# Kernel tuning notes

Measured on AMD Instinct MI355X. Metric: run time of the kernel, lower is better.

The kernel has to match this reference:

```python
import jax, jax.numpy as jnp
import numpy as np

N_WIRES = 8
DIM = 2 ** N_WIRES  # 256
N_OPS = 20

# Fixed realization of tq.RandomLayer(n_ops=20): ops drawn once with a fixed seed.
_rs = np.random.RandomState(0)
RAND_OPS = []
for _ in range(N_OPS):
    k = int(_rs.randint(4))
    if k == 3:
        c, t = _rs.choice(N_WIRES, 2, replace=False)
        RAND_OPS.append(("cnot", int(c), int(t)))
    else:
        RAND_OPS.append((("rx", "ry", "rz")[k], int(_rs.randint(N_WIRES)), 0))

_idx = np.arange(DIM)
# Z eigenvalue sign per wire per basis state (wire 0 = most significant bit)
ZSIGN_NP = np.stack([1.0 - 2.0 * ((_idx >> (N_WIRES - 1 - w)) & 1) for w in range(N_WIRES)]).astype(np.float32)
ZSIGN = jnp.asarray(ZSIGN_NP)        # [8, 256]
ZS_T = jnp.asarray(ZSIGN_NP.T)       # [256, 8]

# CNOT is a basis permutation: precompute index maps for each cnot op.
PERMS = {}
for _i, _op in enumerate(RAND_OPS):
    if _op[0] == "cnot":
        _c, _t = _op[1], _op[2]
        _cb = (_idx >> (N_WIRES - 1 - _c)) & 1
        PERMS[_i] = jnp.asarray(_idx ^ (_cb << (N_WIRES - 1 - _t)))


def _ry_mat(t):
    c = jnp.cos(t * 0.5).astype(jnp.complex64)
    s = jnp.sin(t * 0.5).astype(jnp.complex64)
    return jnp.stack([jnp.stack([c, -s]), jnp.stack([s, c])])


def _rx_mat(t):
    c = jnp.cos(t * 0.5).astype(jnp.complex64)
    s = (-1j * jnp.sin(t * 0.5)).astype(jnp.complex64)
    return jnp.stack([jnp.stack([c, s]), jnp.stack([s, c])])


def _apply_1q(state, U, w):
    # state: [B, 256]; apply 2x2 U on wire w
    B = state.shape[0]
    s = state.reshape(B, 2 ** w, 2, -1)
    return jnp.einsum('ij,bajc->baic', U, s).reshape(B, DIM)


def _forward(x, ry_theta, rand_params, W1, b1, W2, b2):
    B, S, E = x.shape
    f = x.reshape(B * S, E)[:, :N_WIRES]  # encoder uses input_idx 0..7
    # Encoder: RY(f_w) on |0> for each wire -> product state, built by kron chain
    c = jnp.cos(f * 0.5)
    s = jnp.sin(f * 0.5)
    state = jnp.ones((B * S, 1), jnp.float32)
    for w in range(N_WIRES):
        v = jnp.stack([c[:, w], s[:, w]], axis=-1)  # [BS, 2]
        state = (state[:, :, None] * v[:, None, :]).reshape(B * S, -1)
    state = state.astype(jnp.complex64)  # [BS, 256]
    # Fixed random layer
    for i, op in enumerate(RAND_OPS):
        kind = op[0]
        if kind == "cnot":
            state = state[:, PERMS[i]]
        elif kind == "rz":
            ph = jnp.exp((-0.5j * rand_params[i]) * ZSIGN[op[1]]).astype(jnp.complex64)
            state = state * ph[None, :]
        elif kind == "rx":
            state = _apply_1q(state, _rx_mat(rand_params[i]), op[1])
        else:
            state = _apply_1q(state, _ry_mat(rand_params[i]), op[1])
    # Trainable per-wire RY gates
    for w in range(N_WIRES):
        state = _apply_1q(state, _ry_mat(ry_theta[w]), w)
    # MeasureAll(PauliZ): <Z_w> = sum_b |amp_b|^2 * zsign_w(b)
    probs = (state.real ** 2 + state.imag ** 2)  # [BS, 256] float32
    expv = probs @ ZS_T                          # [BS, 8]
    h = jax.nn.relu(expv @ W1.T + b1)
    out = h @ W2.T + b2
    return out.reshape(B, S, -1)


def setup_inputs() -> dict:
    key = jax.random.key(0)
    k1, k2, k3, k4, k5 = jax.random.split(key, 5)
    B, S, E = 4, 4096, 512
    pi = 3.14159265
    x = jax.random.normal(k1, (B, S, E), jnp.float32)
    ry_theta = jax.random.uniform(k2, (N_WIRES,), jnp.float32, -pi, pi)
    rand_params = jax.random.uniform(k3, (N_OPS,), jnp.float32, -pi, pi)
    W1 = jax.random.normal(k4, (64, N_WIRES), jnp.float32) * (1.0 / np.sqrt(N_WIRES))
    b1 = jnp.zeros((64,), jnp.float32)
    W2 = jax.random.normal(k5, (E, 64), jnp.float32) * (1.0 / 8.0)
    b2 = jnp.zeros((E,), jnp.float32)
    return {"x": x, "ry_theta": ry_theta, "rand_params": rand_params, "W1": W1, "b1": b1, "W2": W2, "b2": b2}


def reference(x, ry_theta, rand_params, W1, b1, W2, b2):
    return _forward(x, ry_theta, rand_params, W1, b1, W2, b2)
```

## Files before the change

### kernel.cpp

```cpp
#include <hip/hip_runtime.h>
#include <hip/hip_fp16.h>
#include <cstdint>

#define N_RAND   20
#define N_GATES  28
#define E_DIM    512

struct OpsArg { int d[N_GATES]; };

struct MT19937ce {
  uint32_t mt[624] = {};
  int mti = 0;
  constexpr void seed(uint32_t s){
    mt[0]=s;
    for(int i=1;i<624;i++) mt[i]=1812433253u*(mt[i-1]^(mt[i-1]>>30))+(uint32_t)i;
    mti=624;
  }
  constexpr uint32_t next(){
    if(mti>=624){
      for(int i=0;i<624;i++){
        uint32_t y=(mt[i]&0x80000000u)|(mt[(i+1)%624]&0x7fffffffu);
        mt[i]=mt[(i+397)%624]^(y>>1)^((y&1u)?0x9908b0dfu:0u);
      }
      mti=0;
    }
    uint32_t y=mt[mti++];
    y^=y>>11; y^=(y<<7)&0x9d2c5680u; y^=(y<<15)&0xefc60000u; y^=y>>18;
    return y;
  }
  constexpr uint32_t interval(uint32_t mx){
    if(!mx) return 0;
    uint32_t mask=mx; mask|=mask>>1; mask|=mask>>2; mask|=mask>>4; mask|=mask>>8; mask|=mask>>16;
    uint32_t v = next()&mask;
    while(v>mx) v = next()&mask;
    return v;
  }
};

constexpr OpsArg build_ops_ce(){
  MT19937ce rs; rs.seed(0);
  OpsArg o{};
  for(int i=0;i<N_RAND;i++){
    uint32_t k = rs.interval(3);
    if(k==3){
      int perm[8] = {0,1,2,3,4,5,6,7};
      for(int j=7;j>=1;j--){
        uint32_t t=rs.interval((uint32_t)j);
        int tmp=perm[j]; perm[j]=perm[t]; perm[t]=tmp;
      }
      o.d[i] = 3 | (perm[0]<<2) | (perm[1]<<5);
    } else {
      uint32_t w = rs.interval(7);
      o.d[i] = (int)k | ((int)w<<2);
    }
  }
  for(int i=0;i<8;i++) o.d[N_RAND+i] = 1 | (i<<2);
  return o;
}
inline constexpr OpsArg OPS = build_ops_ce();

__device__ __forceinline__ float readlane_f(float v, int l){
  return __int_as_float(__builtin_amdgcn_readlane(__float_as_int(v), l));
}
template<int CTRL>
__device__ __forceinline__ float dpp_mov(float v){
  int s = __float_as_int(v);
  return __int_as_float(__builtin_amdgcn_update_dpp(s, s, CTRL, 0xF, 0xF, false));
}
template<int M>
__device__ __forceinline__ float xl(float v){
  if constexpr (M==1)      return dpp_mov<0xB1>(v);
  else if constexpr (M==2) return dpp_mov<0x4E>(v);
  else return __int_as_float(__builtin_amdgcn_ds_swizzle(__float_as_int(v), (M<<10)|0x1F));
}
template<int L>
__device__ __forceinline__ float bcast(float v){
  return __int_as_float(__builtin_amdgcn_ds_swizzle(__float_as_int(v), L<<5));
}

typedef _Float16 v2h __attribute__((ext_vector_type(2)));
typedef _Float16 v8h __attribute__((ext_vector_type(8)));
typedef float    v4f __attribute__((ext_vector_type(4)));
union HU  { uint32_t u; v2h h; };

template<int G>
__device__ __forceinline__ void run_gates(float (&ar)[8], float (&ai)[8],
                                          const float (&sgn)[5], int l,
                                          float cv, float sv)
{
  if constexpr (G < N_GATES){
    constexpr int dd   = OPS.d[G];
    constexpr int kind = dd & 3;
    constexpr int wa   = (dd>>2) & 7;
    constexpr int wb   = (dd>>5) & 7;
    const float gc = readlane_f(cv, G);
    const float gs = readlane_f(sv, G);

    if constexpr (kind == 3){
      if constexpr (wa < 3 && wb < 3){
        constexpr int Rc = 4>>wa, Rt = 4>>wb;
        #pragma unroll
        for (int r=0;r<8;r++){
          if ((r & Rc) && !(r & Rt)){
            float t0=ar[r]; ar[r]=ar[r|Rt]; ar[r|Rt]=t0;
            float t1=ai[r]; ai[r]=ai[r|Rt]; ai[r|Rt]=t1;
          }
        }
      } else if constexpr (wa < 3){
        constexpr int Rc = 4>>wa, Mt = 16>>(wb-3);
        #pragma unroll
        for (int r=0;r<8;r++){
          if (r & Rc){ ar[r]=xl<Mt>(ar[r]); ai[r]=xl<Mt>(ai[r]); }
        }
      } else if constexpr (wb < 3){
        constexpr int Mc = 16>>(wa-3), Rt = 4>>wb;
        const bool cb = (l & Mc) != 0;
        #pragma unroll
        for (int r=0;r<8;r++){
          if (!(r & Rt)){
            float alo=ar[r], ahi=ar[r|Rt];
            ar[r]    = cb ? ahi : alo;  ar[r|Rt] = cb ? alo : ahi;
            float blo=ai[r], bhi=ai[r|Rt];
            ai[r]    = cb ? bhi : blo;  ai[r|Rt] = cb ? blo : bhi;
          }
        }
      } else {
        constexpr int Mc = 16>>(wa-3), Mt = 16>>(wb-3);
        const bool cb = (l & Mc) != 0;
        #pragma unroll
        for (int r=0;r<8;r++){
          float pr = xl<Mt>(ar[r]), pi_ = xl<Mt>(ai[r]);
          ar[r] = cb ? pr  : ar[r];
          ai[r] = cb ? pi_ : ai[r];
        }
      }
    } else if constexpr (kind == 2){
      if constexpr (wa < 3){
        constexpr int Rb = 4>>wa;
        #pragma unroll
        for (int r=0;r<8;r++){
          const float pim = (r & Rb) ? gs : -gs;
          float nr = gc*ar[r] - pim*ai[r];
          ai[r] = gc*ai[r] + pim*ar[r];
          ar[r] = nr;
        }
      } else {
        constexpr int SI = wa-3;
        const float pim = sgn[SI]*gs;
        #pragma unroll
        for (int r=0;r<8;r++){
          float nr = gc*ar[r] - pim*ai[r];
          ai[r] = gc*ai[r] + pim*ar[r];
          ar[r] = nr;
        }
      }
    } else if constexpr (kind == 1){
      if constexpr (wa < 3){
        constexpr int Rb = 4>>wa;
        #pragma unroll
        for (int r=0;r<8;r++){
          if (!(r & Rb)){
            const int h = r|Rb;
            float lr=ar[r], li=ai[r], hr=ar[h], hii=ai[h];
            ar[r]=gc*lr - gs*hr;  ai[r]=gc*li - gs*hii;
            ar[h]=gs*lr + gc*hr;  ai[h]=gs*li + gc*hii;
          }
        }
      } else {
        constexpr int M = 16>>(wa-3), SI = wa-3;
        const float sg = sgn[SI]*gs;
        #pragma unroll
        for (int r=0;r<8;r++){
          float pr = xl<M>(ar[r]), pi_ = xl<M>(ai[r]);
          ar[r] = gc*ar[r] + sg*pr;
          ai[r] = gc*ai[r] + sg*pi_;
        }
      }
    } else {
      if constexpr (wa < 3){
        constexpr int Rb = 4>>wa;
        #pragma unroll
        for (int r=0;r<8;r++){
          if (!(r & Rb)){
            const int h = r|Rb;
            float lr=ar[r], li=ai[r], hr=ar[h], hii=ai[h];
            ar[r]=gc*lr + gs*hii;  ai[r]=gc*li - gs*hr;
            ar[h]=gc*hr + gs*li;   ai[h]=gc*hii - gs*lr;
          }
        }
      } else {
        constexpr int M = 16>>(wa-3);
        #pragma unroll
        for (int r=0;r<8;r++){
          float pr = xl<M>(ar[r]), pi_ = xl<M>(ai[r]);
          ar[r] = gc*ar[r] + gs*pi_;
          ai[r] = gc*ai[r] - gs*pr;
        }
      }
    }
    run_gates<G+1>(ar, ai, sgn, l, cv, sv);
  }
}

__global__ __launch_bounds__(512)
void qffb_pre(const float* __restrict__ ry_theta,
              const float* __restrict__ rand_params,
              _Float16* __restrict__ Urf,
              _Float16* __restrict__ Uif)
{
  const int tid  = threadIdx.x;
  const int lane = tid & 63;
  const int l    = lane & 31;
  const int wave = tid >> 6;
  const int b    = blockIdx.x*16 + wave*2 + (lane>>5);

  float th = 0.f;
  if (lane < N_GATES)
    th = (lane < N_RAND) ? rand_params[lane] : ry_theta[lane - N_RAND];
  float cv, sv;
  __sincosf(0.5f*th, &sv, &cv);

  float sgn[5];
  sgn[0] = (l&16) ? 1.f : -1.f;
  sgn[1] = (l& 8) ? 1.f : -1.f;
  sgn[2] = (l& 4) ? 1.f : -1.f;
  sgn[3] = (l& 2) ? 1.f : -1.f;
  sgn[4] = (l& 1) ? 1.f : -1.f;

  float ar[8], ai[8];
  #pragma unroll
  for (int r=0;r<8;r++){
    ar[r] = (((b>>5)==r) && ((b&31)==l)) ? 1.f : 0.f;
    ai[r] = 0.f;
  }

  run_gates<0>(ar, ai, sgn, l, cv, sv);

  const int k  = b >> 5;
  const int qd = (b >> 3) & 3;
  const int jj = b & 7;
  #pragma unroll
  for (int r=0;r<8;r++){
    const int j   = r*32 + l;
    const int nt  = j >> 4;
    const int rr_ = j & 15;
    const size_t F = ((size_t)((nt*8 + k)*4 + qd)*16 + rr_)*8 + jj;
    Urf[F] = (_Float16)ar[r];
    Uif[F] = (_Float16)ai[r];
  }
}

#define PSTRIDE 272
#define PFSTR   264
__global__ __launch_bounds__(512)
void qffb_main(const float* __restrict__ x,
               const _Float16* __restrict__ Urf,
               const _Float16* __restrict__ Uif,
               const float* __restrict__ W1,
               const float* __restrict__ b1,
               const float* __restrict__ W2,
               const float* __restrict__ b2,
               float* __restrict__ out)
{
  __shared__ _Float16 Ps[16*PSTRIDE];
  __shared__ _Float16 Hs[16][72];
  __shared__ float    Ts[8][16*68];
  float* Pf = &Ts[0][0];

  const int tid  = threadIdx.x;
  const int lane = tid & 63;
  const int l    = lane & 31;
  const int wave = tid >> 6;
  const int rr   = lane & 15;
  const int quad = lane >> 4;
  const int trow = wave*2 + (lane>>5);
  const int token = blockIdx.x*16 + trow;

  {
    const float4 xa = *(const float4*)(x + (size_t)token*E_DIM);
    const float4 xb = *(const float4*)(x + (size_t)token*E_DIM + 4);
    float c[8], s[8];
    float xs[8] = {xa.x, xa.y, xa.z, xa.w, xb.x, xb.y, xb.z, xb.w};
    #pragma unroll
    for (int w=0; w<8; ++w) __sincosf(0.5f*xs[w], &s[w], &c[w]);
    float L = ((l&16)? s[0]:c[0]) * ((l&8)? s[1]:c[1]);
    L *= ((l&4)? s[2]:c[2]) * ((l&2)? s[3]:c[3]);
    L *= ((l&1)? s[4]:c[4]);
    const float p67[4] = {c[6]*c[7], c[6]*s[7], s[6]*c[7], s[6]*s[7]};
    v8h v;
    #pragma unroll
    for (int i=0;i<8;++i)
      v[i] = (_Float16)(L * (((i&4)? s[5]:c[5]) * p67[i&3]));
    *(v8h*)&Ps[trow*PSTRIDE + l*8] = v;
  }
  __syncthreads();

  v4f accr[2], acci[2];
  #pragma unroll
  for (int n=0;n<2;++n){ accr[n]=v4f{0.f,0.f,0.f,0.f}; acci[n]=v4f{0.f,0.f,0.f,0.f}; }

  const size_t ub0 = ((size_t)((wave*2+0)*32 + quad)*16 + rr)*8;
  const size_t ub1 = ((size_t)((wave*2+1)*32 + quad)*16 + rr)*8;

  v8h br0 = *(const v8h*)(Urf + ub0);
  v8h bi0 = *(const v8h*)(Uif + ub0);
  v8h br1 = *(const v8h*)(Urf + ub1);
  v8h bi1 = *(const v8h*)(Uif + ub1);

  #pragma unroll
  for (int k=0;k<8;++k){
    v8h nbr0, nbi0, nbr1, nbi1;
    if (k < 7){
      const size_t o = (size_t)(k+1)*512;
      nbr0 = *(const v8h*)(Urf + ub0 + o);
      nbi0 = *(const v8h*)(Uif + ub0 + o);
      nbr1 = *(const v8h*)(Urf + ub1 + o);
      nbi1 = *(const v8h*)(Uif + ub1 + o);
    }
    const v8h a0 = *(const v8h*)&Ps[rr*PSTRIDE + k*32 + quad*8];
    accr[0] = __builtin_amdgcn_mfma_f32_16x16x32_f16(a0, br0, accr[0], 0,0,0);
    acci[0] = __builtin_amdgcn_mfma_f32_16x16x32_f16(a0, bi0, acci[0], 0,0,0);
    accr[1] = __builtin_amdgcn_mfma_f32_16x16x32_f16(a0, br1, accr[1], 0,0,0);
    acci[1] = __builtin_amdgcn_mfma_f32_16x16x32_f16(a0, bi1, acci[1], 0,0,0);
    if (k < 7){ br0=nbr0; bi0=nbi0; br1=nbr1; bi1=nbi1; }
  }

  #pragma unroll
  for (int n=0;n<2;++n){
    const int nt = wave*2 + n;
    #pragma unroll
    for (int r2=0;r2<4;++r2)
      Pf[(quad*4+r2)*PFSTR + nt*16 + rr] =
          accr[n][r2]*accr[n][r2] + acci[n][r2]*acci[n][r2];
  }
  __syncthreads();

  float sgn[5];
  sgn[0] = (l&16) ? 1.f : -1.f;
  sgn[1] = (l& 8) ? 1.f : -1.f;
  sgn[2] = (l& 4) ? 1.f : -1.f;
  sgn[3] = (l& 2) ? 1.f : -1.f;
  sgn[4] = (l& 1) ? 1.f : -1.f;

  float p[8];
  #pragma unroll
  for (int r=0;r<8;r++) p[r] = Pf[trow*PFSTR + r*32 + l];

  const float t1a=p[0]+p[1], t1b=p[2]+p[3], t1c=p[4]+p[5], t1d=p[6]+p[7];
  const float s0a=t1a+t1b, s0b=t1c+t1d;
  float P  = s0a + s0b;
  float e0 = s0a - s0b;
  float e1 = (t1a+t1c) - (t1b+t1d);
  float e2 = (p[0]-p[1])+(p[2]-p[3])+(p[4]-p[5])+(p[6]-p[7]);
  {
    float t;
    t=xl<1>(e0); e0+=t;  t=xl<1>(e1); e1+=t;  t=xl<1>(e2); e2+=t;
    t=xl<1>(P);  P = fmaf(-sgn[4], P, t);
    t=xl<2>(e0); e0+=t;  t=xl<2>(e1); e1+=t;  t=xl<2>(e2); e2+=t;
    t=xl<2>(P);  P = fmaf(-sgn[3], P, t);
    t=xl<4>(e0); e0+=t;  t=xl<4>(e1); e1+=t;  t=xl<4>(e2); e2+=t;
    t=xl<4>(P);  P = fmaf(-sgn[2], P, t);
    t=xl<8>(e0); e0+=t;  t=xl<8>(e1); e1+=t;  t=xl<8>(e2); e2+=t;
    t=xl<8>(P);  P = fmaf(-sgn[1], P, t);
    t=xl<16>(e0); e0+=t; t=xl<16>(e1); e1+=t; t=xl<16>(e2); e2+=t;
    t=xl<16>(P); P = fmaf(-sgn[0], P, t);
  }
  const float e3 = bcast<16>(P);
  const float e4 = bcast<8>(P);
  const float e5 = bcast<4>(P);
  const float e6 = bcast<2>(P);
  const float e7 = bcast<1>(P);

  {
    const float4 wA0 = *(const float4*)(W1 + (size_t)(2*l)*8);
    const float4 wA1 = *(const float4*)(W1 + (size_t)(2*l)*8 + 4);
    const float4 wB0 = *(const float4*)(W1 + (size_t)(2*l+1)*8);
    const float4 wB1 = *(const float4*)(W1 + (size_t)(2*l+1)*8 + 4);
    const float2 bb  = *(const float2*)(b1 + 2*l);
    float h0 = bb.x + wA0.x*e0 + wA0.y*e1 + wA0.z*e2 + wA0.w*e3
                    + wA1.x*e4 + wA1.y*e5 + wA1.z*e6 + wA1.w*e7;
    float h1 = bb.y + wB0.x*e0 + wB0.y*e1 + wB0.z*e2 + wB0.w*e3
                    + wB1.x*e4 + wB1.y*e5 + wB1.z*e6 + wB1.w*e7;
    HU pk;
    pk.h = v2h{(_Float16)fmaxf(h0,0.f), (_Float16)fmaxf(h1,0.f)};
    *(uint32_t*)((char*)&Hs[trow][0] + 4*l) = pk.u;
  }
  __syncthreads();

  const int mt = blockIdx.x;
  const int ng = wave;

  const v8h a0 = *(const v8h*)&Hs[rr][quad*8];
  const v8h a1 = *(const v8h*)&Hs[rr][32 + quad*8];

  #pragma unroll
  for (int j=0;j<4;++j){
    const int e = ng*64 + j*16 + rr;
    const float4 wa = *(const float4*)(W2 + (size_t)e*64 + quad*8);
    const float4 wb = *(const float4*)(W2 + (size_t)e*64 + quad*8 + 4);
    const float4 wc = *(const float4*)(W2 + (size_t)e*64 + 32 + quad*8);
    const float4 wd = *(const float4*)(W2 + (size_t)e*64 + 32 + quad*8 + 4);
    const v8h b0 = v8h{(_Float16)wa.x,(_Float16)wa.y,(_Float16)wa.z,(_Float16)wa.w,
                      (_Float16)wb.x,(_Float16)wb.y,(_Float16)wb.z,(_Float16)wb.w};
    const v8h b1v = v8h{(_Float16)wc.x,(_Float16)wc.y,(_Float16)wc.z,(_Float16)wc.w,
                      (_Float16)wd.x,(_Float16)wd.y,(_Float16)wd.z,(_Float16)wd.w};
    v4f acc = {0.f,0.f,0.f,0.f};
    acc = __builtin_amdgcn_mfma_f32_16x16x32_f16(a0, b0, acc, 0, 0, 0);
    acc = __builtin_amdgcn_mfma_f32_16x16x32_f16(a1, b1v, acc, 0, 0, 0);
    #pragma unroll
    for (int r2=0;r2<4;r2++)
      Ts[wave][(quad*4+r2)*68 + j*16 + rr] = acc[r2];
  }

  const float4 bias = *(const float4*)(b2 + ng*64 + rr*4);
  #pragma unroll
  for (int k=0;k<4;++k){
    const int row = 4*k + quad;
    float4 v = *(const float4*)&Ts[wave][row*68 + rr*4];
    v.x += bias.x; v.y += bias.y; v.z += bias.z; v.w += bias.w;
    const int t = mt*16 + row;
    *(float4*)(out + (size_t)t*E_DIM + ng*64 + rr*4) = v;
  }
}

extern "C" void kernel_launch(void* const* d_in, const int* in_sizes, int n_in,
                              void* d_out, int out_size, void* d_ws, size_t ws_size,
                              hipStream_t stream)
{
  (void)n_in; (void)out_size; (void)ws_size;
  const int ntok = in_sizes[0] / E_DIM;
  char* ws = (char*)d_ws;
  _Float16* Urf = (_Float16*)(ws);
  _Float16* Uif = (_Float16*)(ws + 131072);

  qffb_pre<<<16, 512, 0, stream>>>(
      (const float*)d_in[1],
      (const float*)d_in[2],
      Urf, Uif);

  qffb_main<<<ntok/16, 512, 0, stream>>>(
      (const float*)d_in[0],
      Urf, Uif,
      (const float*)d_in[3],
      (const float*)d_in[4],
      (const float*)d_in[5],
      (const float*)d_in[6],
      (float*)d_out);
}
```

Before: 121.8 us.

## Process four token tiles per block and keep U and W2 in registers

Each block now loops over four 16-token tiles. The unitary B-fragments, W1/b1, the fp16-converted W2 fragments and the b2 bias are loaded once into registers before the loop and reused for every tile. The grid shrinks by four, cutting redundant global loads and fp32-to-fp16 conversion of the weights per block. In exchange register pressure rises considerably, fewer blocks are resident to hide latency, and the tiles inside a block run serially with barriers between stages.

Result: faster. 109.3 us (-10.3%).

```diff
diff --git a/kernel.cpp b/kernel.cpp
--- a/kernel.cpp
+++ b/kernel.cpp
@@ -5,6 +5,7 @@
 #define N_RAND   20
 #define N_GATES  28
 #define E_DIM    512
+#define TPB_TILES 4
 
 struct OpsArg { int d[N_GATES]; };
 
@@ -274,66 +275,18 @@
   const int rr   = lane & 15;
   const int quad = lane >> 4;
   const int trow = wave*2 + (lane>>5);
-  const int token = blockIdx.x*16 + trow;
-
-  {
-    const float4 xa = *(const float4*)(x + (size_t)token*E_DIM);
-    const float4 xb = *(const float4*)(x + (size_t)token*E_DIM + 4);
-    float c[8], s[8];
-    float xs[8] = {xa.x, xa.y, xa.z, xa.w, xb.x, xb.y, xb.z, xb.w};
-    #pragma unroll
-    for (int w=0; w<8; ++w) __sincosf(0.5f*xs[w], &s[w], &c[w]);
-    float L = ((l&16)? s[0]:c[0]) * ((l&8)? s[1]:c[1]);
-    L *= ((l&4)? s[2]:c[2]) * ((l&2)? s[3]:c[3]);
-    L *= ((l&1)? s[4]:c[4]);
-    const float p67[4] = {c[6]*c[7], c[6]*s[7], s[6]*c[7], s[6]*s[7]};
-    v8h v;
-    #pragma unroll
-    for (int i=0;i<8;++i)
-      v[i] = (_Float16)(L * (((i&4)? s[5]:c[5]) * p67[i&3]));
-    *(v8h*)&Ps[trow*PSTRIDE + l*8] = v;
-  }
-  __syncthreads();
-
-  v4f accr[2], acci[2];
-  #pragma unroll
-  for (int n=0;n<2;++n){ accr[n]=v4f{0.f,0.f,0.f,0.f}; acci[n]=v4f{0.f,0.f,0.f,0.f}; }
 
   const size_t ub0 = ((size_t)((wave*2+0)*32 + quad)*16 + rr)*8;
   const size_t ub1 = ((size_t)((wave*2+1)*32 + quad)*16 + rr)*8;
-
-  v8h br0 = *(const v8h*)(Urf + ub0);
-  v8h bi0 = *(const v8h*)(Uif + ub0);
-  v8h br1 = *(const v8h*)(Urf + ub1);
-  v8h bi1 = *(const v8h*)(Uif + ub1);
-
+  v8h Br0[8], Bi0[8], Br1[8], Bi1[8];
   #pragma unroll
   for (int k=0;k<8;++k){
-    v8h nbr0, nbi0, nbr1, nbi1;
-    if (k < 7){
-      const size_t o = (size_t)(k+1)*512;
-      nbr0 = *(const v8h*)(Urf + ub0 + o);
-      nbi0 = *(const v8h*)(Uif + ub0 + o);
-      nbr1 = *(const v8h*)(Urf + ub1 + o);
-      nbi1 = *(const v8h*)(Uif + ub1 + o);
-    }
-    const v8h a0 = *(const v8h*)&Ps[rr*PSTRIDE + k*32 + quad*8];
-    accr[0] = __builtin_amdgcn_mfma_f32_16x16x32_f16(a0, br0, accr[0], 0,0,0);
-    acci[0] = __builtin_amdgcn_mfma_f32_16x16x32_f16(a0, bi0, acci[0], 0,0,0);
-    accr[1] = __builtin_amdgcn_mfma_f32_16x16x32_f16(a0, br1, accr[1], 0,0,0);
-    acci[1] = __builtin_amdgcn_mfma_f32_16x16x32_f16(a0, bi1, acci[1], 0,0,0);
-    if (k < 7){ br0=nbr0; bi0=nbi0; br1=nbr1; bi1=nbi1; }
-  }
-
-  #pragma unroll
-  for (int n=0;n<2;++n){
-    const int nt = wave*2 + n;
-    #pragma unroll
-    for (int r2=0;r2<4;++r2)
-      Pf[(quad*4+r2)*PFSTR + nt*16 + rr] =
-          accr[n][r2]*accr[n][r2] + acci[n][r2]*acci[n][r2];
-  }
-  __syncthreads();
+    const size_t o = (size_t)k*512;
+    Br0[k] = *(const v8h*)(Urf + ub0 + o);
+    Bi0[k] = *(const v8h*)(Uif + ub0 + o);
+    Br1[k] = *(const v8h*)(Urf + ub1 + o);
+    Bi1[k] = *(const v8h*)(Uif + ub1 + o);
+  }
 
   float sgn[5];
   sgn[0] = (l&16) ? 1.f : -1.f;
@@ -342,57 +295,14 @@
   sgn[3] = (l& 2) ? 1.f : -1.f;
   sgn[4] = (l& 1) ? 1.f : -1.f;
 
-  float p[8];
-  #pragma unroll
-  for (int r=0;r<8;r++) p[r] = Pf[trow*PFSTR + r*32 + l];
-
-  const float t1a=p[0]+p[1], t1b=p[2]+p[3], t1c=p[4]+p[5], t1d=p[6]+p[7];
-  const float s0a=t1a+t1b, s0b=t1c+t1d;
-  float P  = s0a + s0b;
-  float e0 = s0a - s0b;
-  float e1 = (t1a+t1c) - (t1b+t1d);
-  float e2 = (p[0]-p[1])+(p[2]-p[3])+(p[4]-p[5])+(p[6]-p[7]);
-  {
-    float t;
-    t=xl<1>(e0); e0+=t;  t=xl<1>(e1); e1+=t;  t=xl<1>(e2); e2+=t;
-    t=xl<1>(P);  P = fmaf(-sgn[4], P, t);
-    t=xl<2>(e0); e0+=t;  t=xl<2>(e1); e1+=t;  t=xl<2>(e2); e2+=t;
-    t=xl<2>(P);  P = fmaf(-sgn[3], P, t);
-    t=xl<4>(e0); e0+=t;  t=xl<4>(e1); e1+=t;  t=xl<4>(e2); e2+=t;
-    t=xl<4>(P);  P = fmaf(-sgn[2], P, t);
-    t=xl<8>(e0); e0+=t;  t=xl<8>(e1); e1+=t;  t=xl<8>(e2); e2+=t;
-    t=xl<8>(P);  P = fmaf(-sgn[1], P, t);
-    t=xl<16>(e0); e0+=t; t=xl<16>(e1); e1+=t; t=xl<16>(e2); e2+=t;
-    t=xl<16>(P); P = fmaf(-sgn[0], P, t);
-  }
-  const float e3 = bcast<16>(P);
-  const float e4 = bcast<8>(P);
-  const float e5 = bcast<4>(P);
-  const float e6 = bcast<2>(P);
-  const float e7 = bcast<1>(P);
-
-  {
-    const float4 wA0 = *(const float4*)(W1 + (size_t)(2*l)*8);
-    const float4 wA1 = *(const float4*)(W1 + (size_t)(2*l)*8 + 4);
-    const float4 wB0 = *(const float4*)(W1 + (size_t)(2*l+1)*8);
-    const float4 wB1 = *(const float4*)(W1 + (size_t)(2*l+1)*8 + 4);
-    const float2 bb  = *(const float2*)(b1 + 2*l);
-    float h0 = bb.x + wA0.x*e0 + wA0.y*e1 + wA0.z*e2 + wA0.w*e3
-                    + wA1.x*e4 + wA1.y*e5 + wA1.z*e6 + wA1.w*e7;
-    float h1 = bb.y + wB0.x*e0 + wB0.y*e1 + wB0.z*e2 + wB0.w*e3
-                    + wB1.x*e4 + wB1.y*e5 + wB1.z*e6 + wB1.w*e7;
-    HU pk;
-    pk.h = v2h{(_Float16)fmaxf(h0,0.f), (_Float16)fmaxf(h1,0.f)};
-    *(uint32_t*)((char*)&Hs[trow][0] + 4*l) = pk.u;
-  }
-  __syncthreads();
-
-  const int mt = blockIdx.x;
+  const float4 wA0 = *(const float4*)(W1 + (size_t)(2*l)*8);
+  const float4 wA1 = *(const float4*)(W1 + (size_t)(2*l)*8 + 4);
+  const float4 wB0 = *(const float4*)(W1 + (size_t)(2*l+1)*8);
+  const float4 wB1 = *(const float4*)(W1 + (size_t)(2*l+1)*8 + 4);
+  const float2 bb  = *(const float2*)(b1 + 2*l);
+
   const int ng = wave;
-
-  const v8h a0 = *(const v8h*)&Hs[rr][quad*8];
-  const v8h a1 = *(const v8h*)&Hs[rr][32 + quad*8];
-
+  v8h WB0[4], WB1[4];
   #pragma unroll
   for (int j=0;j<4;++j){
     const int e = ng*64 + j*16 + rr;
@@ -400,26 +310,122 @@
     const float4 wb = *(const float4*)(W2 + (size_t)e*64 + quad*8 + 4);
     const float4 wc = *(const float4*)(W2 + (size_t)e*64 + 32 + quad*8);
     const float4 wd = *(const float4*)(W2 + (size_t)e*64 + 32 + quad*8 + 4);
-    const v8h b0 = v8h{(_Float16)wa.x,(_Float16)wa.y,(_Float16)wa.z,(_Float16)wa.w,
-                      (_Float16)wb.x,(_Float16)wb.y,(_Float16)wb.z,(_Float16)wb.w};
-    const v8h b1v = v8h{(_Float16)wc.x,(_Float16)wc.y,(_Float16)wc.z,(_Float16)wc.w,
-                      (_Float16)wd.x,(_Float16)wd.y,(_Float16)wd.z,(_Float16)wd.w};
-    v4f acc = {0.f,0.f,0.f,0.f};
-    acc = __builtin_amdgcn_mfma_f32_16x16x32_f16(a0, b0, acc, 0, 0, 0);
-    acc = __builtin_amdgcn_mfma_f32_16x16x32_f16(a1, b1v, acc, 0, 0, 0);
+    WB0[j] = v8h{(_Float16)wa.x,(_Float16)wa.y,(_Float16)wa.z,(_Float16)wa.w,
+                 (_Float16)wb.x,(_Float16)wb.y,(_Float16)wb.z,(_Float16)wb.w};
+    WB1[j] = v8h{(_Float16)wc.x,(_Float16)wc.y,(_Float16)wc.z,(_Float16)wc.w,
+                 (_Float16)wd.x,(_Float16)wd.y,(_Float16)wd.z,(_Float16)wd.w};
+  }
+  const float4 bias = *(const float4*)(b2 + ng*64 + rr*4);
+
+  for (int it=0; it<TPB_TILES; ++it){
+    const int tileIdx = blockIdx.x*TPB_TILES + it;
+    const int token   = tileIdx*16 + trow;
+
+    {
+      const float4 xa = *(const float4*)(x + (size_t)token*E_DIM);
+      const float4 xb = *(const float4*)(x + (size_t)token*E_DIM + 4);
+      float c[8], s[8];
+      float xs[8] = {xa.x, xa.y, xa.z, xa.w, xb.x, xb.y, xb.z, xb.w};
+      #pragma unroll
+      for (int w=0; w<8; ++w) __sincosf(0.5f*xs[w], &s[w], &c[w]);
+      float L = ((l&16)? s[0]:c[0]) * ((l&8)? s[1]:c[1]);
+      L *= ((l&4)? s[2]:c[2]) * ((l&2)? s[3]:c[3]);
+      L *= ((l&1)? s[4]:c[4]);
+      const float p67[4] = {c[6]*c[7], c[6]*s[7], s[6]*c[7], s[6]*s[7]};
+      v8h v;
+      #pragma unroll
+      for (int i=0;i<8;++i)
+        v[i] = (_Float16)(L * (((i&4)? s[5]:c[5]) * p67[i&3]));
+      *(v8h*)&Ps[trow*PSTRIDE + l*8] = v;
+    }
+    __syncthreads();
+
+    v4f accr[2], acci[2];
     #pragma unroll
-    for (int r2=0;r2<4;r2++)
-      Ts[wave][(quad*4+r2)*68 + j*16 + rr] = acc[r2];
-  }
-
-  const float4 bias = *(const float4*)(b2 + ng*64 + rr*4);
-  #pragma unroll
-  for (int k=0;k<4;++k){
-    const int row = 4*k + quad;
-    float4 v = *(const float4*)&Ts[wave][row*68 + rr*4];
-    v.x += bias.x; v.y += bias.y; v.z += bias.z; v.w += bias.w;
-    const int t = mt*16 + row;
-    *(float4*)(out + (size_t)t*E_DIM + ng*64 + rr*4) = v;
+    for (int n=0;n<2;++n){ accr[n]=v4f{0.f,0.f,0.f,0.f}; acci[n]=v4f{0.f,0.f,0.f,0.f}; }
+
+    #pragma unroll
+    for (int k=0;k<8;++k){
+      const v8h a0 = *(const v8h*)&Ps[rr*PSTRIDE + k*32 + quad*8];
+      accr[0] = __builtin_amdgcn_mfma_f32_16x16x32_f16(a0, Br0[k], accr[0], 0,0,0);
+      acci[0] = __builtin_amdgcn_mfma_f32_16x16x32_f16(a0, Bi0[k], acci[0], 0,0,0);
+      accr[1] = __builtin_amdgcn_mfma_f32_16x16x32_f16(a0, Br1[k], accr[1], 0,0,0);
+      acci[1] = __builtin_amdgcn_mfma_f32_16x16x32_f16(a0, Bi1[k], acci[1], 0,0,0);
+    }
+
+    #pragma unroll
+    for (int n=0;n<2;++n){
+      const int nt = wave*2 + n;
+      #pragma unroll
+      for (int r2=0;r2<4;++r2)
+        Pf[(quad*4+r2)*PFSTR + nt*16 + rr] =
+            accr[n][r2]*accr[n][r2] + acci[n][r2]*acci[n][r2];
+    }
+    __syncthreads();
+
+    {
+      float p[8];
+      #pragma unroll
+      for (int r=0;r<8;r++) p[r] = Pf[trow*PFSTR + r*32 + l];
+
+      const float t1a=p[0]+p[1], t1b=p[2]+p[3], t1c=p[4]+p[5], t1d=p[6]+p[7];
+      const float s0a=t1a+t1b, s0b=t1c+t1d;
+      float P  = s0a + s0b;
+      float e0 = s0a - s0b;
+      float e1 = (t1a+t1c) - (t1b+t1d);
+      float e2 = (p[0]-p[1])+(p[2]-p[3])+(p[4]-p[5])+(p[6]-p[7]);
+      {
+        float t;
+        t=xl<1>(e0); e0+=t;  t=xl<1>(e1); e1+=t;  t=xl<1>(e2); e2+=t;
+        t=xl<1>(P);  P = fmaf(-sgn[4], P, t);
+        t=xl<2>(e0); e0+=t;  t=xl<2>(e1); e1+=t;  t=xl<2>(e2); e2+=t;
+        t=xl<2>(P);  P = fmaf(-sgn[3], P, t);
+        t=xl<4>(e0); e0+=t;  t=xl<4>(e1); e1+=t;  t=xl<4>(e2); e2+=t;
+        t=xl<4>(P);  P = fmaf(-sgn[2], P, t);
+        t=xl<8>(e0); e0+=t;  t=xl<8>(e1); e1+=t;  t=xl<8>(e2); e2+=t;
+        t=xl<8>(P);  P = fmaf(-sgn[1], P, t);
+        t=xl<16>(e0); e0+=t; t=xl<16>(e1); e1+=t; t=xl<16>(e2); e2+=t;
+        t=xl<16>(P); P = fmaf(-sgn[0], P, t);
+      }
+      const float e3 = bcast<16>(P);
+      const float e4 = bcast<8>(P);
+      const float e5 = bcast<4>(P);
+      const float e6 = bcast<2>(P);
+      const float e7 = bcast<1>(P);
+
+      float h0 = bb.x + wA0.x*e0 + wA0.y*e1 + wA0.z*e2 + wA0.w*e3
+                      + wA1.x*e4 + wA1.y*e5 + wA1.z*e6 + wA1.w*e7;
+      float h1 = bb.y + wB0.x*e0 + wB0.y*e1 + wB0.z*e2 + wB0.w*e3
+                      + wB1.x*e4 + wB1.y*e5 + wB1.z*e6 + wB1.w*e7;
+      HU pk;
+      pk.h = v2h{(_Float16)fmaxf(h0,0.f), (_Float16)fmaxf(h1,0.f)};
+      *(uint32_t*)((char*)&Hs[trow][0] + 4*l) = pk.u;
+    }
+    __syncthreads();
+
+    {
+      const v8h a0 = *(const v8h*)&Hs[rr][quad*8];
+      const v8h a1 = *(const v8h*)&Hs[rr][32 + quad*8];
+
+      #pragma unroll
+      for (int j=0;j<4;++j){
+        v4f acc = {0.f,0.f,0.f,0.f};
+        acc = __builtin_amdgcn_mfma_f32_16x16x32_f16(a0, WB0[j], acc, 0, 0, 0);
+        acc = __builtin_amdgcn_mfma_f32_16x16x32_f16(a1, WB1[j], acc, 0, 0, 0);
+        #pragma unroll
+        for (int r2=0;r2<4;r2++)
+          Ts[wave][(quad*4+r2)*68 + j*16 + rr] = acc[r2];
+      }
+
+      #pragma unroll
+      for (int k=0;k<4;++k){
+        const int row = 4*k + quad;
+        float4 v = *(const float4*)&Ts[wave][row*68 + rr*4];
+        v.x += bias.x; v.y += bias.y; v.z += bias.z; v.w += bias.w;
+        const int t = tileIdx*16 + row;
+        *(float4*)(out + (size_t)t*E_DIM + ng*64 + rr*4) = v;
+      }
+    }
   }
 }
 
@@ -438,7 +444,7 @@
       (const float*)d_in[2],
       Urf, Uif);
 
-  qffb_main<<<ntok/16, 512, 0, stream>>>(
+  qffb_main<<<ntok/16/TPB_TILES, 512, 0, stream>>>(
       (const float*)d_in[0],
       Urf, Uif,
       (const float*)d_in[3],
```
